# Kernel tuning notes

Measured on AMD Instinct MI355X. Metric: run time of the kernel, lower is better.

## Reference

```python
import jax, jax.numpy as jnp
import numpy as np

NUM_EXPERTS = 8
TOP_K = 2
P_NORM = 1.0  # moe_normalize_expert_weights
HIDDEN = 1024
FFN_HIDDEN = 2048
BATCH, SEQ = 2, 2048


def setup_inputs() -> dict:
    key = jax.random.key(0)
    ks = jax.random.split(key, 5)
    s = 0.02
    return {
        "x": jax.random.normal(ks[0], (BATCH, SEQ, HIDDEN), dtype=jnp.float32),
        "router_w": jax.random.normal(ks[1], (NUM_EXPERTS, HIDDEN), dtype=jnp.float32) * s,
        "w1": jax.random.normal(ks[2], (NUM_EXPERTS, FFN_HIDDEN, HIDDEN), dtype=jnp.float32) * s,
        "v1": jax.random.normal(ks[3], (NUM_EXPERTS, FFN_HIDDEN, HIDDEN), dtype=jnp.float32) * s,
        "w2": jax.random.normal(ks[4], (NUM_EXPERTS, FFN_HIDDEN, HIDDEN), dtype=jnp.float32) * s,
    }


def reference(x, router_w, w1, v1, w2):
    B, S, H = x.shape
    xf = x.reshape(-1, H)  # [T, H]

    # Router: softmax in fp32, top-k, L-p normalize, cast back.
    logits = xf @ router_w.T  # [T, E]
    probs = jax.nn.softmax(logits.astype(jnp.float32), axis=-1)
    top_w, top_e = jax.lax.top_k(probs, TOP_K)  # [T, K]
    norm = jnp.sum(jnp.abs(top_w) ** P_NORM, axis=-1, keepdims=True) ** (1.0 / P_NORM)
    top_w = (top_w / norm).astype(x.dtype)

    # Per-token combine weight for each expert: c[t,e] = sum_k top_w[t,k]*[top_e[t,k]==e]
    c = jnp.sum(jax.nn.one_hot(top_e, NUM_EXPERTS, dtype=x.dtype) * top_w[..., None], axis=1)  # [T, E]

    # Dense per-expert GLU; routing realized by output gating with c (zero for unrouted tokens).
    out = jnp.zeros_like(xf)
    for e in range(NUM_EXPERTS):
        h = jax.nn.silu(xf @ w1[e].T) * (xf @ v1[e].T)  # [T, F]
        out = out + (h @ w2[e]) * c[:, e:e + 1]  # [T, H]
    return out.reshape(B, S, H)
```

## Files before the change

kernel.cpp:

```cpp
#include <hip/hip_runtime.h>
#include <stdint.h>

#define T_TOKENS 4096
#define HID 1024
#define FFN 2048
#define NE 8

typedef __attribute__((ext_vector_type(8))) short bf16x8;
typedef __attribute__((ext_vector_type(4))) float f32x4;

__device__ __forceinline__ unsigned short f2bf(float f) {
  union { float f; uint32_t u; } v; v.f = f;
  uint32_t r = v.u + 0x7FFFu + ((v.u >> 16) & 1u);
  return (unsigned short)(r >> 16);
}

__device__ __forceinline__ uint32_t pack2(float a, float b) {
  return (uint32_t)f2bf(a) | ((uint32_t)f2bf(b) << 16);
}

__device__ __forceinline__ float bf2f(uint32_t lo16) {
  union { uint32_t u; float f; } v; v.u = lo16 << 16; return v.f;
}

__device__ __forceinline__ void gload16(const unsigned short* g, unsigned short* l) {
  __builtin_amdgcn_global_load_lds(
      (const __attribute__((address_space(1))) void*)(g),
      (__attribute__((address_space(3))) void*)(l), 16, 0, 0);
}

__device__ __forceinline__ int frag_off(int r, int g) {
  return r * 32 + ((g ^ ((r >> 1) & 3)) << 3);
}

constexpr size_t XBF_OFF  = 0;
constexpr size_t HBUF_OFF = (size_t)T_TOKENS * HID * 2;
constexpr size_t TOKE_OFF = HBUF_OFF + (size_t)T_TOKENS * 2 * FFN * 2;
constexpr size_t TOKW_OFF = TOKE_OFF + (size_t)T_TOKENS * 2 * 4;
constexpr size_t CNT_OFF  = TOKW_OFF + (size_t)T_TOKENS * 2 * 4;
constexpr size_t OFF_OFF  = CNT_OFF + 64;
constexpr size_t LIST_OFF = OFF_OFF + 64;
constexpr size_t META_END = LIST_OFF + (size_t)NE * T_TOKENS * 4;
constexpr size_t PB1_OFF  = META_END;
constexpr size_t PB2_OFF  = PB1_OFF + (size_t)NE * FFN * HID * 2;
constexpr size_t PW2_OFF  = PB2_OFF + (size_t)NE * FFN * HID * 2;
constexpr size_t WS_BIG   = PW2_OFF + (size_t)NE * HID * FFN * 2;
constexpr size_t YBUF_OFF = PB1_OFF;

__global__ __launch_bounds__(256) void pack_w1v1_kernel(const float* __restrict__ w1,
                                                        const float* __restrict__ v1,
                                                        unsigned short* __restrict__ pb1,
                                                        unsigned short* __restrict__ pb2) {
  int colblk = blockIdx.x;
  int kslab  = blockIdx.y;
  int ez     = blockIdx.z;
  const float* src = (ez < NE) ? w1 : v1;
  unsigned short* dst = (ez < NE) ? pb1 : pb2;
  int e = ez & (NE - 1);
  __shared__ unsigned short lds[2048];
  int t = threadIdx.x;
  int c  = colblk * 16 + (t >> 4);
  int k0 = kslab * 128 + (t & 15) * 8;
  const float* sp = src + ((size_t)e * FFN + c) * HID + k0;
  float4 a = *(const float4*)sp;
  float4 b = *(const float4*)(sp + 4);
  uint4 o;
  o.x = pack2(a.x, a.y); o.y = pack2(a.z, a.w);
  o.z = pack2(b.x, b.y); o.w = pack2(b.z, b.w);
  int chunk = ((t & 15) >> 2) * 64 + ((t & 3) * 16 + (t >> 4));
  int pos = chunk ^ ((chunk >> 4) & 15);
  *(uint4*)(lds + pos * 8) = o;
  __syncthreads();
  int rpos = t ^ ((t >> 4) & 15);
  uint4 v = *(const uint4*)(lds + rpos * 8);
  unsigned short* dp = dst + (((size_t)e * (FFN / 16) + colblk) * (HID / 32) + kslab * 4) * 512 + t * 8;
  *(uint4*)dp = v;
}

__global__ __launch_bounds__(256) void pack_w2_kernel(const float* __restrict__ w2,
                                                      unsigned short* __restrict__ pw2) {
  int cb = blockIdx.x;
  int kb = blockIdx.y;
  int e  = blockIdx.z;
  __shared__ unsigned short s[64][68];
  int t = threadIdx.x;
  int tr = t >> 4, tc = (t & 15) * 4;
  const float* src = w2 + ((size_t)e * FFN + kb * 64) * HID + cb * 64;
#pragma unroll
  for (int i = 0; i < 4; ++i) {
    int k = tr + i * 16;
    float4 v = *(const float4*)(src + (size_t)k * HID + tc);
    s[k][tc + 0] = f2bf(v.x); s[k][tc + 1] = f2bf(v.y);
    s[k][tc + 2] = f2bf(v.z); s[k][tc + 3] = f2bf(v.w);
  }
  __syncthreads();
#pragma unroll
  for (int half = 0; half < 2; ++half) {
    int cid = t + half * 256;
    int colblk_l = cid >> 7;
    int ks_l = (cid >> 6) & 1;
    int lane = cid & 63;
    unsigned short tmp[8];
#pragma unroll
    for (int j = 0; j < 8; ++j)
      tmp[j] = s[ks_l * 32 + (lane >> 4) * 8 + j][colblk_l * 16 + (lane & 15)];
    uint4 o;
    o.x = tmp[0] | (tmp[1] << 16); o.y = tmp[2] | (tmp[3] << 16);
    o.z = tmp[4] | (tmp[5] << 16); o.w = tmp[6] | (tmp[7] << 16);
    unsigned short* dp = pw2 + (((size_t)e * (HID / 16) + cb * 4 + colblk_l) * (FFN / 32)
                                + kb * 2 + ks_l) * 512 + lane * 8;
    *(uint4*)dp = o;
  }
}

__global__ __launch_bounds__(256) void router_kernel(const float* __restrict__ x,
                                                     const float* __restrict__ rw,
                                                     int* __restrict__ tok_e,
                                                     float* __restrict__ tok_w,
                                                     unsigned short* __restrict__ xbf) {
  __shared__ float s_rw[NE * HID];
  int tid = threadIdx.x;
  for (int i = tid; i < NE * HID / 4; i += 256)
    ((float4*)s_rw)[i] = ((const float4*)rw)[i];
  __syncthreads();
  int wave = tid >> 6, lane = tid & 63;
  int t = blockIdx.x * 4 + wave;
  const float* xr = x + (size_t)t * HID;
  unsigned short* xbr = xbf + (size_t)t * HID;
  float acc[NE];
#pragma unroll
  for (int e = 0; e < NE; ++e) acc[e] = 0.0f;
#pragma unroll
  for (int c = 0; c < HID / 256; ++c) {
    int idx = c * 256 + lane * 4;
    float4 xv = *(const float4*)(xr + idx);
    uint2 pk; pk.x = pack2(xv.x, xv.y); pk.y = pack2(xv.z, xv.w);
    *(uint2*)(xbr + idx) = pk;
#pragma unroll
    for (int e = 0; e < NE; ++e) {
      float4 rv = *(const float4*)(s_rw + e * HID + idx);
      acc[e] += xv.x * rv.x + xv.y * rv.y + xv.z * rv.z + xv.w * rv.w;
    }
  }
#pragma unroll
  for (int e = 0; e < NE; ++e)
    for (int off = 32; off > 0; off >>= 1) acc[e] += __shfl_down(acc[e], off);
  if (lane == 0) {
    float m = acc[0];
#pragma unroll
    for (int e = 1; e < NE; ++e) m = fmaxf(m, acc[e]);
    float p[NE], Z = 0.0f;
#pragma unroll
    for (int e = 0; e < NE; ++e) { p[e] = expf(acc[e] - m); Z += p[e]; }
    int e0 = 0;
#pragma unroll
    for (int e = 1; e < NE; ++e) if (p[e] > p[e0]) e0 = e;
    int e1 = (e0 == 0) ? 1 : 0;
#pragma unroll
    for (int e = 0; e < NE; ++e) if (e != e0 && p[e] > p[e1]) e1 = e;
    float w0 = p[e0] / Z, w1 = p[e1] / Z;
    float nrm = w0 + w1;
    tok_e[t * 2] = e0; tok_e[t * 2 + 1] = e1;
    tok_w[t * 2] = w0 / nrm; tok_w[t * 2 + 1] = w1 / nrm;
  }
}

__global__ __launch_bounds__(1024) void scatter_offsets_kernel(
    const int* __restrict__ tok_e, int* __restrict__ counts,
    int* __restrict__ offs, int* __restrict__ lists) {
  __shared__ int c[NE];
  int tid = threadIdx.x;
  if (tid < NE) c[tid] = 0;
  __syncthreads();
  for (int p = tid; p < T_TOKENS * 2; p += 1024) {
    int e = tok_e[p];
    int pos = atomicAdd(&c[e], 1);
    lists[e * T_TOKENS + pos] = p;
  }
  __syncthreads();
  if (tid == 0) {
    int r = 0;
    for (int e = 0; e < NE; ++e) { counts[e] = c[e]; offs[e] = r; r += c[e]; }
  }
}

__global__ __launch_bounds__(256) void combine_kernel(const unsigned short* __restrict__ ybuf,
                                                      float* __restrict__ out) {
  int t = blockIdx.x;
  int c = threadIdx.x;
  uint2 ua = *(const uint2*)(ybuf + (size_t)(2 * t) * HID + c * 4);
  uint2 ub = *(const uint2*)(ybuf + (size_t)(2 * t + 1) * HID + c * 4);
  float4 r;
  r.x = bf2f(ua.x & 0xffff) + bf2f(ub.x & 0xffff);
  r.y = bf2f(ua.x >> 16)    + bf2f(ub.x >> 16);
  r.z = bf2f(ua.y & 0xffff) + bf2f(ub.y & 0xffff);
  r.w = bf2f(ua.y >> 16)    + bf2f(ub.y >> 16);
  ((float4*)(out + (size_t)t * HID))[c] = r;
}

__global__ __launch_bounds__(512) void gemm1b_kernel(
    const unsigned short* __restrict__ xbf,
    const unsigned short* __restrict__ pb1, const unsigned short* __restrict__ pb2,
    const int* __restrict__ counts, const int* __restrict__ offs,
    const int* __restrict__ lists, unsigned short* __restrict__ hbuf) {
  constexpr int ABUF = 128 * 32;
  constexpr int BBUF = 128 * 32;
  constexpr int NT = HID / 32;
  int nt = blockIdx.x, mt = blockIdx.y, e = blockIdx.z;
  int ne = counts[e];
  if (mt * 128 >= ne) return;
  __shared__ unsigned short s_a[2 * ABUF];
  __shared__ unsigned short s_b1[2 * BBUF];
  int tid = threadIdx.x;
  int srow = tid >> 2, slot = tid & 3;
  int lchunk = slot ^ ((srow >> 1) & 3);
  const int* lst = lists + e * T_TOKENS + mt * 128;
  int tok = lst[(mt * 128 + srow < ne) ? srow : 0] >> 1;
  const unsigned short* aptr = xbf + (size_t)tok * HID + lchunk * 8;
  int g8 = tid >> 6, ln = tid & 63;
  const unsigned short* b1p =
      pb1 + ((size_t)(e * (FFN / 16) + nt * 8 + g8) * (HID / 32)) * 512 + ln * 8;

  int lane = tid & 63, wv = tid >> 6;
  int wm = (wv >> 2) * 64, wn = (wv & 3) * 32;
  int rl = lane & 15, g = lane >> 4;
  int aoff[4];
#pragma unroll
  for (int m = 0; m < 4; ++m) aoff[m] = frag_off(wm + m * 16 + rl, g);
  int b1off[2];
#pragma unroll
  for (int n = 0; n < 2; ++n) b1off[n] = (((wv & 3) * 2 + n) * 64 + lane) * 8;
  size_t cb2 = (size_t)e * (FFN / 16) + nt * 8 + (wv & 3) * 2;
  const unsigned short* p2_0 = pb2 + (cb2 + 0) * (HID / 32) * 512 + lane * 8;
  const unsigned short* p2_1 = pb2 + (cb2 + 1) * (HID / 32) * 512 + lane * 8;

  f32x4 zero = {0.0f, 0.0f, 0.0f, 0.0f};
  f32x4 acc1[4][2], acc2[4][2];
#pragma unroll
  for (int i = 0; i < 4; ++i)
#pragma unroll
    for (int j = 0; j < 2; ++j) { acc1[i][j] = zero; acc2[i][j] = zero; }

  auto stage = [&](int s, int t) {
    gload16(aptr + t * 32, s_a + s * ABUF + tid * 8);
    gload16(b1p + (size_t)t * 512, s_b1 + s * BBUF + tid * 8);
  };
  bf16x8 b2X[2], b2Y[2];
  auto loadBX = [&](int t) {
    b2X[0] = *(const bf16x8*)(p2_0 + (size_t)t * 512);
    b2X[1] = *(const bf16x8*)(p2_1 + (size_t)t * 512);
  };
  auto loadBY = [&](int t) {
    b2Y[0] = *(const bf16x8*)(p2_0 + (size_t)t * 512);
    b2Y[1] = *(const bf16x8*)(p2_1 + (size_t)t * 512);
  };
  auto compute = [&](int s, bf16x8 (&b2)[2]) {
    const unsigned short* pa = s_a + s * ABUF;
    const unsigned short* pb = s_b1 + s * BBUF;
    bf16x8 af[4], bf1[2];
#pragma unroll
    for (int m = 0; m < 4; ++m) af[m] = *(const bf16x8*)(pa + aoff[m]);
#pragma unroll
    for (int n = 0; n < 2; ++n) bf1[n] = *(const bf16x8*)(pb + b1off[n]);
#pragma unroll
    for (int m = 0; m < 4; ++m)
#pragma unroll
      for (int n = 0; n < 2; ++n) {
        acc1[m][n] = __builtin_amdgcn_mfma_f32_16x16x32_bf16(af[m], bf1[n], acc1[m][n], 0, 0, 0);
        acc2[m][n] = __builtin_amdgcn_mfma_f32_16x16x32_bf16(af[m], b2[n], acc2[m][n], 0, 0, 0);
      }
  };

  stage(0, 0);
  loadBX(0);
  __syncthreads();
  for (int t = 0; t < NT; t += 2) {
    stage(1, t + 1);
    loadBY(t + 1);
    compute(0, b2X);
    __syncthreads();
    if (t + 2 < NT) { stage(0, t + 2); loadBX(t + 2); }
    compute(1, b2Y);
    __syncthreads();
  }

  int hb = offs[e];
#pragma unroll
  for (int m = 0; m < 4; ++m) {
#pragma unroll
    for (int j = 0; j < 4; ++j) {
      int r = mt * 128 + wm + m * 16 + (lane >> 4) * 4 + j;
      if (r < ne) {
        size_t rowo = (size_t)(hb + r) * FFN;
#pragma unroll
        for (int n = 0; n < 2; ++n) {
          int col = nt * 128 + wn + n * 16 + rl;
          float c1 = acc1[m][n][j], c2 = acc2[m][n][j];
          float h = c1 / (1.0f + __expf(-c1)) * c2;
          hbuf[rowo + col] = f2bf(h);
        }
      }
    }
  }
}

__global__ __launch_bounds__(512) void gemm2b_kernel(
    const unsigned short* __restrict__ hbuf, const unsigned short* __restrict__ pw2,
    const int* __restrict__ counts, const int* __restrict__ offs,
    const int* __restrict__ lists, const float* __restrict__ tok_w,
    unsigned short* __restrict__ ybuf) {
  constexpr int BUFSZ = 128 * 32;
  constexpr int NT = FFN / 32;
  int nt = blockIdx.x, mt = blockIdx.y, e = blockIdx.z;
  int ne = counts[e];
  if (mt * 128 >= ne) return;
  __shared__ unsigned short s_a[2 * BUFSZ];
  int tid = threadIdx.x;
  int hb = offs[e];
  int srow = tid >> 2, slot = tid & 3;
  int lchunk = slot ^ ((srow >> 1) & 3);
  int ar = mt * 128 + ((mt * 128 + srow < ne) ? srow : 0);
  const unsigned short* aptr = hbuf + (size_t)(hb + ar) * FFN + lchunk * 8;

  int lane = tid & 63, wv = tid >> 6;
  int wm = (wv >> 2) * 64, wn = (wv & 3) * 32;
  int rl = lane & 15, g = lane >> 4;
  int aoff[4];
#pragma unroll
  for (int m = 0; m < 4; ++m) aoff[m] = frag_off(wm + m * 16 + rl, g);

  size_t cb = (size_t)e * (HID / 16) + nt * 8 + (wv & 3) * 2;
  const unsigned short* p_0 = pw2 + (cb + 0) * (FFN / 32) * 512 + lane * 8;
  const unsigned short* p_1 = pw2 + (cb + 1) * (FFN / 32) * 512 + lane * 8;

  f32x4 zero = {0.0f, 0.0f, 0.0f, 0.0f};
  f32x4 acc[4][2];
#pragma unroll
  for (int i = 0; i < 4; ++i)
#pragma unroll
    for (int j = 0; j < 2; ++j) acc[i][j] = zero;

  auto stageA = [&](int s, int t) {
    gload16(aptr + t * 32, s_a + s * BUFSZ + tid * 8);
  };
  bf16x8 bX[2], bY[2];
  auto loadBX = [&](int t) {
    bX[0] = *(const bf16x8*)(p_0 + (size_t)t * 512);
    bX[1] = *(const bf16x8*)(p_1 + (size_t)t * 512);
  };
  auto loadBY = [&](int t) {
    bY[0] = *(const bf16x8*)(p_0 + (size_t)t * 512);
    bY[1] = *(const bf16x8*)(p_1 + (size_t)t * 512);
  };
  auto compute = [&](int s, bf16x8 (&b)[2]) {
    const unsigned short* pa = s_a + s * BUFSZ;
    bf16x8 af[4];
#pragma unroll
    for (int m = 0; m < 4; ++m) af[m] = *(const bf16x8*)(pa + aoff[m]);
#pragma unroll
    for (int m = 0; m < 4; ++m)
#pragma unroll
      for (int n = 0; n < 2; ++n)
        acc[m][n] = __builtin_amdgcn_mfma_f32_16x16x32_bf16(af[m], b[n], acc[m][n], 0, 0, 0);
  };

  stageA(0, 0);
  loadBX(0);
  __syncthreads();
  for (int t = 0; t < NT; t += 2) {
    stageA(1, t + 1);
    loadBY(t + 1);
    compute(0, bX);
    __syncthreads();
    if (t + 2 < NT) { stageA(0, t + 2); loadBX(t + 2); }
    compute(1, bY);
    __syncthreads();
  }

#pragma unroll
  for (int m = 0; m < 4; ++m) {
#pragma unroll
    for (int j = 0; j < 4; ++j) {
      int r = mt * 128 + wm + m * 16 + (lane >> 4) * 4 + j;
      if (r < ne) {
        int p = lists[e * T_TOKENS + r];
        float w = tok_w[p];
        unsigned short* yrow = ybuf + (size_t)p * HID;
#pragma unroll
        for (int n = 0; n < 2; ++n) {
          int col = nt * 128 + wn + n * 16 + rl;
          yrow[col] = f2bf(acc[m][n][j] * w);
        }
      }
    }
  }
}


__global__ __launch_bounds__(512) void gemm1_kernel(
    const unsigned short* __restrict__ xbf,
    const float* __restrict__ w1, const float* __restrict__ v1,
    const int* __restrict__ counts, const int* __restrict__ offs,
    const int* __restrict__ lists, unsigned short* __restrict__ hbuf) {
  int nt = blockIdx.x, mt = blockIdx.y, e = blockIdx.z;
  int ne = counts[e];
  if (mt * 128 >= ne) return;
  int nrows = ne - mt * 128; if (nrows > 128) nrows = 128;
  __shared__ unsigned short s_a[128 * 40];
  __shared__ unsigned short s_b1[128 * 40];
  __shared__ unsigned short s_b2[128 * 40];
  const int* lst = lists + e * T_TOKENS + mt * 128;
  int tid = threadIdx.x;
  int sr = tid >> 2, sc = tid & 3;
  int pr = lst[(sr < nrows) ? sr : 0];
  const unsigned short* asrc = xbf + (size_t)(pr >> 1) * HID + sc * 8;
  size_t brow = ((size_t)e * FFN + nt * 128 + sr) * HID + sc * 8;
  const float* b1s = w1 + brow;
  const float* b2s = v1 + brow;
  int lane = tid & 63, wv = tid >> 6;
  int wm = (wv >> 2) * 64, wn = (wv & 3) * 32;
  int rl = lane & 15, kg = (lane >> 4) * 8;
  f32x4 zero = {0.0f, 0.0f, 0.0f, 0.0f};
  f32x4 acc1[4][2], acc2[4][2];
#pragma unroll
  for (int i = 0; i < 4; ++i)
#pragma unroll
    for (int j = 0; j < 2; ++j) { acc1[i][j] = zero; acc2[i][j] = zero; }
  int sdst = sr * 40 + sc * 8;
  for (int kk = 0; kk < HID; kk += 32) {
    uint4 av = *(const uint4*)(asrc + kk);
    float4 f0 = *(const float4*)(b1s + kk);
    float4 f1 = *(const float4*)(b1s + kk + 4);
    float4 g0 = *(const float4*)(b2s + kk);
    float4 g1 = *(const float4*)(b2s + kk + 4);
    *(uint4*)(s_a + sdst) = av;
    uint4 bv; bv.x = pack2(f0.x, f0.y); bv.y = pack2(f0.z, f0.w);
    bv.z = pack2(f1.x, f1.y); bv.w = pack2(f1.z, f1.w);
    *(uint4*)(s_b1 + sdst) = bv;
    uint4 cv; cv.x = pack2(g0.x, g0.y); cv.y = pack2(g0.z, g0.w);
    cv.z = pack2(g1.x, g1.y); cv.w = pack2(g1.z, g1.w);
    *(uint4*)(s_b2 + sdst) = cv;
    __syncthreads();
    bf16x8 af[4], bf1[2], bf2[2];
#pragma unroll
    for (int m = 0; m < 4; ++m)
      af[m] = *(const bf16x8*)(s_a + (wm + m * 16 + rl) * 40 + kg);
#pragma unroll
    for (int n = 0; n < 2; ++n) {
      bf1[n] = *(const bf16x8*)(s_b1 + (wn + n * 16 + rl) * 40 + kg);
      bf2[n] = *(const bf16x8*)(s_b2 + (wn + n * 16 + rl) * 40 + kg);
    }
#pragma unroll
    for (int m = 0; m < 4; ++m)
#pragma unroll
      for (int n = 0; n < 2; ++n) {
        acc1[m][n] = __builtin_amdgcn_mfma_f32_16x16x32_bf16(af[m], bf1[n], acc1[m][n], 0, 0, 0);
        acc2[m][n] = __builtin_amdgcn_mfma_f32_16x16x32_bf16(af[m], bf2[n], acc2[m][n], 0, 0, 0);
      }
    __syncthreads();
  }
  int hb = offs[e];
#pragma unroll
  for (int m = 0; m < 4; ++m) {
#pragma unroll
    for (int j = 0; j < 4; ++j) {
      int r = mt * 128 + wm + m * 16 + (lane >> 4) * 4 + j;
      if (r < ne) {
        size_t rowo = (size_t)(hb + r) * FFN;
#pragma unroll
        for (int n = 0; n < 2; ++n) {
          int col = nt * 128 + wn + n * 16 + rl;
          float c1 = acc1[m][n][j], c2 = acc2[m][n][j];
          float h = c1 / (1.0f + __expf(-c1)) * c2;
          hbuf[rowo + col] = f2bf(h);
        }
      }
    }
  }
}

__global__ __launch_bounds__(512) void gemm2_kernel(
    const unsigned short* __restrict__ hbuf, const float* __restrict__ w2,
    const int* __restrict__ counts, const int* __restrict__ offs,
    const int* __restrict__ lists, const float* __restrict__ tok_w,
    float* __restrict__ out) {
  int nt = blockIdx.x, mt = blockIdx.y, e = blockIdx.z;
  int ne = counts[e];
  if (mt * 128 >= ne) return;
  int nrows = ne - mt * 128; if (nrows > 128) nrows = 128;
  __shared__ unsigned short s_a[128 * 40];
  __shared__ unsigned short s_b[128 * 40];
  int tid = threadIdx.x;
  int hb = offs[e];
  int sr = tid >> 2, sc = tid & 3;
  int ar = mt * 128 + ((sr < nrows) ? sr : 0);
  const unsigned short* asrc = hbuf + (size_t)(hb + ar) * FFN + sc * 8;
  int bk = tid >> 4, bn = tid & 15;
  const float* bsrc = w2 + ((size_t)e * FFN + bk) * HID + nt * 128 + bn;
  int lane = tid & 63, wv = tid >> 6;
  int wm = (wv >> 2) * 64, wn = (wv & 3) * 32;
  int rl = lane & 15, kg = (lane >> 4) * 8;
  f32x4 zero = {0.0f, 0.0f, 0.0f, 0.0f};
  f32x4 acc[4][2];
#pragma unroll
  for (int i = 0; i < 4; ++i)
#pragma unroll
    for (int j = 0; j < 2; ++j) acc[i][j] = zero;
  int sdst = sr * 40 + sc * 8;
  for (int kk = 0; kk < FFN; kk += 32) {
    uint4 av = *(const uint4*)(asrc + kk);
    const float* bs = bsrc + (size_t)kk * HID;
    float bvals[8];
#pragma unroll
    for (int i = 0; i < 8; ++i) bvals[i] = bs[i * 16];
    *(uint4*)(s_a + sdst) = av;
#pragma unroll
    for (int i = 0; i < 8; ++i) s_b[(bn + i * 16) * 40 + bk] = f2bf(bvals[i]);
    __syncthreads();
    bf16x8 af[4], bfr[2];
#pragma unroll
    for (int m = 0; m < 4; ++m)
      af[m] = *(const bf16x8*)(s_a + (wm + m * 16 + rl) * 40 + kg);
#pragma unroll
    for (int n = 0; n < 2; ++n)
      bfr[n] = *(const bf16x8*)(s_b + (wn + n * 16 + rl) * 40 + kg);
#pragma unroll
    for (int m = 0; m < 4; ++m)
#pragma unroll
      for (int n = 0; n < 2; ++n)
        acc[m][n] = __builtin_amdgcn_mfma_f32_16x16x32_bf16(af[m], bfr[n], acc[m][n], 0, 0, 0);
    __syncthreads();
  }
#pragma unroll
  for (int m = 0; m < 4; ++m) {
#pragma unroll
    for (int j = 0; j < 4; ++j) {
      int r = mt * 128 + wm + m * 16 + (lane >> 4) * 4 + j;
      if (r < ne) {
        int p = lists[e * T_TOKENS + r];
        float w = tok_w[p];
        float* orow = out + (size_t)(p >> 1) * HID;
#pragma unroll
        for (int n = 0; n < 2; ++n) {
          int col = nt * 128 + wn + n * 16 + rl;
          atomicAdd(orow + col, acc[m][n][j] * w);
        }
      }
    }
  }
}

extern "C" void kernel_launch(void* const* d_in, const int* in_sizes, int n_in,
                              void* d_out, int out_size, void* d_ws, size_t ws_size,
                              hipStream_t stream) {
  const float* x  = (const float*)d_in[0];
  const float* rw = (const float*)d_in[1];
  const float* w1 = (const float*)d_in[2];
  const float* v1 = (const float*)d_in[3];
  const float* w2 = (const float*)d_in[4];
  float* out = (float*)d_out;
  char* ws = (char*)d_ws;
  if (ws_size < META_END) return;

  unsigned short* xbf  = (unsigned short*)(ws + XBF_OFF);
  unsigned short* hbuf = (unsigned short*)(ws + HBUF_OFF);
  int*   tok_e  = (int*)(ws + TOKE_OFF);
  float* tok_w  = (float*)(ws + TOKW_OFF);
  int*   counts = (int*)(ws + CNT_OFF);
  int*   offs   = (int*)(ws + OFF_OFF);
  int*   lists  = (int*)(ws + LIST_OFF);

  router_kernel<<<T_TOKENS / 4, 256, 0, stream>>>(x, rw, tok_e, tok_w, xbf);
  scatter_offsets_kernel<<<1, 1024, 0, stream>>>(tok_e, counts, offs, lists);

  if (ws_size >= WS_BIG) {
    unsigned short* pb1 = (unsigned short*)(ws + PB1_OFF);
    unsigned short* pb2 = (unsigned short*)(ws + PB2_OFF);
    unsigned short* pw2 = (unsigned short*)(ws + PW2_OFF);
    unsigned short* ybuf = (unsigned short*)(ws + YBUF_OFF);
    pack_w1v1_kernel<<<dim3(FFN / 16, HID / 128, 2 * NE), 256, 0, stream>>>(w1, v1, pb1, pb2);
    pack_w2_kernel<<<dim3(HID / 64, FFN / 64, NE), 256, 0, stream>>>(w2, pw2);
    gemm1b_kernel<<<dim3(FFN / 128, T_TOKENS / 128, NE), 512, 0, stream>>>(
        xbf, pb1, pb2, counts, offs, lists, hbuf);
    gemm2b_kernel<<<dim3(HID / 128, T_TOKENS / 128, NE), 512, 0, stream>>>(
        hbuf, pw2, counts, offs, lists, tok_w, ybuf);
    combine_kernel<<<T_TOKENS, 256, 0, stream>>>(ybuf, out);
  } else {
    hipMemsetAsync(d_out, 0, (size_t)T_TOKENS * HID * 4, stream);
    gemm1_kernel<<<dim3(FFN / 128, T_TOKENS / 128, NE), 512, 0, stream>>>(
        xbf, w1, v1, counts, offs, lists, hbuf);
    gemm2_kernel<<<dim3(HID / 128, T_TOKENS / 128, NE), 512, 0, stream>>>(
        hbuf, w2, counts, offs, lists, tok_w, out);
  }
}
```

Before: 245.0 us.

## Fuse router into w1/v1 pack launch and w2 pack into gemm1 grid

The router computation is merged into the w1/v1 packing kernel as an extra grid slice, and the w2 packing is merged into the gemm1 kernel as extra z-slices. This cuts two kernel launches and lets weight conversion overlap with routing and the first GEMM instead of running serially. In exchange, the pack blocks carry the router's larger shared-memory allocation (32KB), which may lower occupancy, and w2 packing now competes with gemm1 for compute units.

```diff
diff --git a/kernel.cpp b/kernel.cpp
--- a/kernel.cpp
+++ b/kernel.cpp
@@ -47,69 +47,84 @@
 constexpr size_t WS_BIG   = PW2_OFF + (size_t)NE * HID * FFN * 2;
 constexpr size_t YBUF_OFF = PB1_OFF;
 
-__global__ __launch_bounds__(256) void pack_w1v1_kernel(const float* __restrict__ w1,
-                                                        const float* __restrict__ v1,
-                                                        unsigned short* __restrict__ pb1,
-                                                        unsigned short* __restrict__ pb2) {
-  int colblk = blockIdx.x;
-  int kslab  = blockIdx.y;
-  int ez     = blockIdx.z;
-  const float* src = (ez < NE) ? w1 : v1;
-  unsigned short* dst = (ez < NE) ? pb1 : pb2;
-  int e = ez & (NE - 1);
-  __shared__ unsigned short lds[2048];
+__global__ __launch_bounds__(256) void pack_router_kernel(
+    const float* __restrict__ w1, const float* __restrict__ v1,
+    unsigned short* __restrict__ pb1, unsigned short* __restrict__ pb2,
+    const float* __restrict__ x, const float* __restrict__ rw,
+    int* __restrict__ tok_e, float* __restrict__ tok_w,
+    unsigned short* __restrict__ xbf) {
+  __shared__ float smem[NE * HID];
+  int z = blockIdx.z;
   int t = threadIdx.x;
-  int c  = colblk * 16 + (t >> 4);
-  int k0 = kslab * 128 + (t & 15) * 8;
-  const float* sp = src + ((size_t)e * FFN + c) * HID + k0;
-  float4 a = *(const float4*)sp;
-  float4 b = *(const float4*)(sp + 4);
-  uint4 o;
-  o.x = pack2(a.x, a.y); o.y = pack2(a.z, a.w);
-  o.z = pack2(b.x, b.y); o.w = pack2(b.z, b.w);
-  int chunk = ((t & 15) >> 2) * 64 + ((t & 3) * 16 + (t >> 4));
-  int pos = chunk ^ ((chunk >> 4) & 15);
-  *(uint4*)(lds + pos * 8) = o;
+  if (z < 2 * NE) {
+    unsigned short* lds = (unsigned short*)smem;
+    int colblk = blockIdx.x;
+    int kslab  = blockIdx.y;
+    const float* src = (z < NE) ? w1 : v1;
+    unsigned short* dst = (z < NE) ? pb1 : pb2;
+    int e = z & (NE - 1);
+    int c  = colblk * 16 + (t >> 4);
+    int k0 = kslab * 128 + (t & 15) * 8;
+    const float* sp = src + ((size_t)e * FFN + c) * HID + k0;
+    float4 a = *(const float4*)sp;
+    float4 b = *(const float4*)(sp + 4);
+    uint4 o;
+    o.x = pack2(a.x, a.y); o.y = pack2(a.z, a.w);
+    o.z = pack2(b.x, b.y); o.w = pack2(b.z, b.w);
+    int chunk = ((t & 15) >> 2) * 64 + ((t & 3) * 16 + (t >> 4));
+    int pos = chunk ^ ((chunk >> 4) & 15);
+    *(uint4*)(lds + pos * 8) = o;
+    __syncthreads();
+    int rpos = t ^ ((t >> 4) & 15);
+    uint4 v = *(const uint4*)(lds + rpos * 8);
+    unsigned short* dp = dst + (((size_t)e * (FFN / 16) + colblk) * (HID / 32) + kslab * 4) * 512 + t * 8;
+    *(uint4*)dp = v;
+    return;
+  }
+  float* s_rw = smem;
+  for (int i = t; i < NE * HID / 4; i += 256)
+    ((float4*)s_rw)[i] = ((const float4*)rw)[i];
   __syncthreads();
-  int rpos = t ^ ((t >> 4) & 15);
-  uint4 v = *(const uint4*)(lds + rpos * 8);
-  unsigned short* dp = dst + (((size_t)e * (FFN / 16) + colblk) * (HID / 32) + kslab * 4) * 512 + t * 8;
-  *(uint4*)dp = v;
-}
-
-__global__ __launch_bounds__(256) void pack_w2_kernel(const float* __restrict__ w2,
-                                                      unsigned short* __restrict__ pw2) {
-  int cb = blockIdx.x;
-  int kb = blockIdx.y;
-  int e  = blockIdx.z;
-  __shared__ unsigned short s[64][68];
-  int t = threadIdx.x;
-  int tr = t >> 4, tc = (t & 15) * 4;
-  const float* src = w2 + ((size_t)e * FFN + kb * 64) * HID + cb * 64;
-#pragma unroll
-  for (int i = 0; i < 4; ++i) {
-    int k = tr + i * 16;
-    float4 v = *(const float4*)(src + (size_t)k * HID + tc);
-    s[k][tc + 0] = f2bf(v.x); s[k][tc + 1] = f2bf(v.y);
-    s[k][tc + 2] = f2bf(v.z); s[k][tc + 3] = f2bf(v.w);
-  }
-  __syncthreads();
-#pragma unroll
-  for (int half = 0; half < 2; ++half) {
-    int cid = t + half * 256;
-    int colblk_l = cid >> 7;
-    int ks_l = (cid >> 6) & 1;
-    int lane = cid & 63;
-    unsigned short tmp[8];
-#pragma unroll
-    for (int j = 0; j < 8; ++j)
-      tmp[j] = s[ks_l * 32 + (lane >> 4) * 8 + j][colblk_l * 16 + (lane & 15)];
-    uint4 o;
-    o.x = tmp[0] | (tmp[1] << 16); o.y = tmp[2] | (tmp[3] << 16);
-    o.z = tmp[4] | (tmp[5] << 16); o.w = tmp[6] | (tmp[7] << 16);
-    unsigned short* dp = pw2 + (((size_t)e * (HID / 16) + cb * 4 + colblk_l) * (FFN / 32)
-                                + kb * 2 + ks_l) * 512 + lane * 8;
-    *(uint4*)dp = o;
+  int rblk = blockIdx.x * 8 + blockIdx.y;
+  int wave = t >> 6, lane = t & 63;
+  int tok = rblk * 4 + wave;
+  const float* xr = x + (size_t)tok * HID;
+  unsigned short* xbr = xbf + (size_t)tok * HID;
+  float acc[NE];
+#pragma unroll
+  for (int e = 0; e < NE; ++e) acc[e] = 0.0f;
+#pragma unroll
+  for (int c = 0; c < HID / 256; ++c) {
+    int idx = c * 256 + lane * 4;
+    float4 xv = *(const float4*)(xr + idx);
+    uint2 pk; pk.x = pack2(xv.x, xv.y); pk.y = pack2(xv.z, xv.w);
+    *(uint2*)(xbr + idx) = pk;
+#pragma unroll
+    for (int e = 0; e < NE; ++e) {
+      float4 rv = *(const float4*)(s_rw + e * HID + idx);
+      acc[e] += xv.x * rv.x + xv.y * rv.y + xv.z * rv.z + xv.w * rv.w;
+    }
+  }
+#pragma unroll
+  for (int e = 0; e < NE; ++e)
+    for (int off = 32; off > 0; off >>= 1) acc[e] += __shfl_down(acc[e], off);
+  if (lane == 0) {
+    float m = acc[0];
+#pragma unroll
+    for (int e = 1; e < NE; ++e) m = fmaxf(m, acc[e]);
+    float p[NE], Z = 0.0f;
+#pragma unroll
+    for (int e = 0; e < NE; ++e) { p[e] = expf(acc[e] - m); Z += p[e]; }
+    int e0 = 0;
+#pragma unroll
+    for (int e = 1; e < NE; ++e) if (p[e] > p[e0]) e0 = e;
+    int e1 = (e0 == 0) ? 1 : 0;
+#pragma unroll
+    for (int e = 0; e < NE; ++e) if (e != e0 && p[e] > p[e1]) e1 = e;
+    float w0 = p[e0] / Z, w1 = p[e1] / Z;
+    float nrm = w0 + w1;
+    tok_e[tok * 2] = e0; tok_e[tok * 2 + 1] = e1;
+    tok_w[tok * 2] = w0 / nrm; tok_w[tok * 2 + 1] = w1 / nrm;
   }
 }
 
@@ -198,20 +213,53 @@
   ((float4*)(out + (size_t)t * HID))[c] = r;
 }
 
-__global__ __launch_bounds__(512) void gemm1b_kernel(
+__global__ __launch_bounds__(512) void gemm1_packw2_kernel(
     const unsigned short* __restrict__ xbf,
     const unsigned short* __restrict__ pb1, const unsigned short* __restrict__ pb2,
     const int* __restrict__ counts, const int* __restrict__ offs,
-    const int* __restrict__ lists, unsigned short* __restrict__ hbuf) {
+    const int* __restrict__ lists, unsigned short* __restrict__ hbuf,
+    const float* __restrict__ w2, unsigned short* __restrict__ pw2) {
   constexpr int ABUF = 128 * 32;
   constexpr int BBUF = 128 * 32;
   constexpr int NT = HID / 32;
-  int nt = blockIdx.x, mt = blockIdx.y, e = blockIdx.z;
+  __shared__ unsigned short s_a[2 * ABUF];
+  __shared__ unsigned short s_b1[2 * BBUF];
+  int z = blockIdx.z;
+  int tid = threadIdx.x;
+
+  if (z >= NE) {
+    unsigned short (*s)[68] = (unsigned short (*)[68])s_a;
+    int e2 = z - NE;
+    int cb = blockIdx.x;
+    int kb = blockIdx.y;
+    const float* src = w2 + ((size_t)e2 * FFN + kb * 64) * HID + cb * 64;
+#pragma unroll
+    for (int i = 0; i < 2; ++i) {
+      int fid = tid + i * 512;
+      int k = fid >> 4;
+      int c4 = (fid & 15) * 4;
+      float4 v = *(const float4*)(src + (size_t)k * HID + c4);
+      s[k][c4 + 0] = f2bf(v.x); s[k][c4 + 1] = f2bf(v.y);
+      s[k][c4 + 2] = f2bf(v.z); s[k][c4 + 3] = f2bf(v.w);
+    }
+    __syncthreads();
+    int colblk_l = tid >> 7, ks_l = (tid >> 6) & 1, lane = tid & 63;
+    unsigned short tmp[8];
+#pragma unroll
+    for (int j = 0; j < 8; ++j)
+      tmp[j] = s[ks_l * 32 + (lane >> 4) * 8 + j][colblk_l * 16 + (lane & 15)];
+    uint4 o;
+    o.x = tmp[0] | (tmp[1] << 16); o.y = tmp[2] | (tmp[3] << 16);
+    o.z = tmp[4] | (tmp[5] << 16); o.w = tmp[6] | (tmp[7] << 16);
+    unsigned short* dp = pw2 + (((size_t)e2 * (HID / 16) + cb * 4 + colblk_l) * (FFN / 32)
+                                + kb * 2 + ks_l) * 512 + lane * 8;
+    *(uint4*)dp = o;
+    return;
+  }
+
+  int nt = blockIdx.x, mt = blockIdx.y, e = z;
   int ne = counts[e];
   if (mt * 128 >= ne) return;
-  __shared__ unsigned short s_a[2 * ABUF];
-  __shared__ unsigned short s_b1[2 * BBUF];
-  int tid = threadIdx.x;
   int srow = tid >> 2, slot = tid & 3;
   int lchunk = slot ^ ((srow >> 1) & 3);
   const int* lst = lists + e * T_TOKENS + mt * 128;
@@ -570,22 +618,22 @@
   int*   offs   = (int*)(ws + OFF_OFF);
   int*   lists  = (int*)(ws + LIST_OFF);
 
-  router_kernel<<<T_TOKENS / 4, 256, 0, stream>>>(x, rw, tok_e, tok_w, xbf);
-  scatter_offsets_kernel<<<1, 1024, 0, stream>>>(tok_e, counts, offs, lists);
-
   if (ws_size >= WS_BIG) {
     unsigned short* pb1 = (unsigned short*)(ws + PB1_OFF);
     unsigned short* pb2 = (unsigned short*)(ws + PB2_OFF);
     unsigned short* pw2 = (unsigned short*)(ws + PW2_OFF);
     unsigned short* ybuf = (unsigned short*)(ws + YBUF_OFF);
-    pack_w1v1_kernel<<<dim3(FFN / 16, HID / 128, 2 * NE), 256, 0, stream>>>(w1, v1, pb1, pb2);
-    pack_w2_kernel<<<dim3(HID / 64, FFN / 64, NE), 256, 0, stream>>>(w2, pw2);
-    gemm1b_kernel<<<dim3(FFN / 128, T_TOKENS / 128, NE), 512, 0, stream>>>(
-        xbf, pb1, pb2, counts, offs, lists, hbuf);
+    pack_router_kernel<<<dim3(FFN / 16, HID / 128, 2 * NE + 1), 256, 0, stream>>>(
+        w1, v1, pb1, pb2, x, rw, tok_e, tok_w, xbf);
+    scatter_offsets_kernel<<<1, 1024, 0, stream>>>(tok_e, counts, offs, lists);
+    gemm1_packw2_kernel<<<dim3(FFN / 128, T_TOKENS / 128, 2 * NE), 512, 0, stream>>>(
+        xbf, pb1, pb2, counts, offs, lists, hbuf, w2, pw2);
     gemm2b_kernel<<<dim3(HID / 128, T_TOKENS / 128, NE), 512, 0, stream>>>(
         hbuf, pw2, counts, offs, lists, tok_w, ybuf);
     combine_kernel<<<T_TOKENS, 256, 0, stream>>>(ybuf, out);
   } else {
+    router_kernel<<<T_TOKENS / 4, 256, 0, stream>>>(x, rw, tok_e, tok_w, xbf);
+    scatter_offsets_kernel<<<1, 1024, 0, stream>>>(tok_e, counts, offs, lists);
     hipMemsetAsync(d_out, 0, (size_t)T_TOKENS * HID * 4, stream);
     gemm1_kernel<<<dim3(FFN / 128, T_TOKENS / 128, NE), 512, 0, stream>>>(
         xbf, w1, v1, counts, offs, lists, hbuf);
```

New measurement: 230.0 us (median of 2 runs). -6.1%, faster.
